# Optimization experiments

Measured on AMD Instinct MI355X. Metric: run time of the kernel, lower is better.

The kernel has to match this reference:

```python
import jax, jax.numpy as jnp
import numpy as np
from jax import lax

K = 3      # kernel_size
C = 64     # n_feat
B, H, W = 2, 256, 256


def _conv(x, w, b, pad):
    # NCHW conv, stride 1
    out = lax.conv_general_dilated(x, w, (1, 1), [(pad, pad), (pad, pad)],
                                   dimension_numbers=('NCHW', 'OIHW', 'NCHW'))
    return out + b[None, :, None, None]


def _prelu(x, a):
    # nn.PReLU() with a single shared learnable slope (init 0.25)
    return jnp.where(x >= 0, x, a * x)


def setup_inputs():
    key = jax.random.key(0)
    ks = jax.random.split(key, 20)
    s = 0.05
    def w(k, shape):
        return jax.random.normal(k, shape, jnp.float32) * s
    inp = {
        'image': jax.random.normal(ks[0], (B, C, H, W), jnp.float32),
        'guidance': jax.random.normal(ks[1], (B, C, H, W), jnp.float32),
        # self.tensor: 1x1 conv (2C -> C) + PReLU (shared with jbf_conv's act)
        'tensor_w': w(ks[2], (C, 2 * C, 1, 1)),
        'tensor_b': jnp.zeros((C,), jnp.float32),
        'a_jbf': jnp.full((1,), 0.25, jnp.float32),
        'kg_w1': w(ks[3], (C, C, 3, 3)), 'kg_b1': jnp.zeros((C,), jnp.float32),
        'kg_w2': w(ks[4], (C, C, 3, 3)), 'kg_b2': jnp.zeros((C,), jnp.float32),
        'kg_w3': w(ks[5], (C, C, 3, 3)), 'kg_b3': jnp.zeros((C,), jnp.float32),
        'kg_w4': w(ks[6], (C, C, 3, 3)), 'kg_b4': jnp.zeros((C,), jnp.float32),
        'kg_w5': w(ks[7], (K * K * C, C, 1, 1)),
        'kg_b5': jnp.zeros((K * K * C,), jnp.float32),
        'a_kg': jnp.full((1,), 0.25, jnp.float32),
        # jbf_conv: 3x3 C->C, PReLU (shared a_jbf), 3x3 C->C
        'jbf_w1': w(ks[8], (C, C, 3, 3)), 'jbf_b1': jnp.zeros((C,), jnp.float32),
        'jbf_w2': w(ks[9], (C, C, 3, 3)), 'jbf_b2': jnp.zeros((C,), jnp.float32),
    }
    return inp


def reference(image, guidance, tensor_w, tensor_b, a_jbf,
              kg_w1, kg_b1, kg_w2, kg_b2, kg_w3, kg_b3, kg_w4, kg_b4,
              kg_w5, kg_b5, a_kg, jbf_w1, jbf_b1, jbf_w2, jbf_b2):
    b, c, h, w = image.shape
    # fuse target+guidance features
    t = _prelu(_conv(jnp.concatenate([image, guidance], axis=1), tensor_w, tensor_b, 0), a_jbf)
    # concat_kg: predict per-pixel dynamic kernel (b, K*K*c, h, w)
    y = t
    for wt, bs in ((kg_w1, kg_b1), (kg_w2, kg_b2), (kg_w3, kg_b3), (kg_w4, kg_b4)):
        y = _prelu(_conv(y, wt, bs, 1), a_kg)
    bi_kernel = _conv(y, kg_w5, kg_b5, 0)
    # unfold: torch layout is channel-major (c, ki, kj) along dim 1
    p = (K - 1) // 2
    xp = jnp.pad(image, ((0, 0), (0, 0), (p, p), (p, p)))
    taps = [xp[:, :, i:i + h, j:j + w] for i in range(K) for j in range(K)]
    patch = jnp.stack(taps, axis=2).reshape(b, c * K * K, h, w)
    # NOTE: faithful to source -- (c*K*K) flat layout reinterpreted as (K*K, c)
    jbf = (patch * bi_kernel).reshape(b, K * K, c, h, w).sum(axis=1)
    out = _conv(_prelu(_conv(jbf, jbf_w1, jbf_b1, 1), a_jbf), jbf_w2, jbf_b2, 1)
    return out + image
```

## Files before the change

### kernel.cpp

```cpp
#include <hip/hip_runtime.h>

#define HW 65536

typedef __bf16 bf16x8 __attribute__((ext_vector_type(8)));
typedef float f32x16 __attribute__((ext_vector_type(16)));

__device__ inline unsigned short f2bf(float x) {
    union { float f; unsigned u; } v; v.f = x;
    unsigned r = v.u + 0x7FFF + ((v.u >> 16) & 1);
    return (unsigned short)(r >> 16);
}
__device__ inline float bfhi2f(unsigned u) {
    union { unsigned u; float f; } v; v.u = u & 0xffff0000u; return v.f;
}
__device__ inline float bflo2f(unsigned u) {
    union { unsigned u; float f; } v; v.u = u << 16; return v.f;
}

union FragU { uint4 u; bf16x8 v; };
__device__ inline bf16x8 ld_frag(const uint4* p) { FragU t; t.u = *p; return t.v; }

__global__ __launch_bounds__(256) void k_wprep(
    const float* __restrict__ w0, const float* __restrict__ w1,
    const float* __restrict__ w2, const float* __restrict__ w3,
    const float* __restrict__ w4, const float* __restrict__ w5,
    const float* __restrict__ w5c, const float* __restrict__ tw,
    unsigned short* __restrict__ wT)
{
    int y = blockIdx.y;
    unsigned short* o = wT + (size_t)y * 36864;
    if (y < 6) {
        const float* ws_[6] = {w0, w1, w2, w3, w4, w5};
        const float* w = ws_[y];
        for (int e = blockIdx.x * 256 + threadIdx.x; e < 36864; e += gridDim.x * 256) {
            int tap = e >> 12, oc = (e >> 6) & 63, ic = e & 63;
            o[e] = f2bf(w[(oc * 64 + ic) * 9 + tap]);
        }
    } else if (y == 6) {
        for (int e = blockIdx.x * 256 + threadIdx.x; e < 36864; e += gridDim.x * 256)
            o[e] = f2bf(w5c[e]);
    } else {
        for (int e = blockIdx.x * 256 + threadIdx.x; e < 8192; e += gridDim.x * 256)
            o[e] = f2bf(tw[e]);
    }
}

__global__ __launch_bounds__(256) void k_tr(
    const float* __restrict__ img, const float* __restrict__ gd,
    unsigned short* __restrict__ imgT, unsigned short* __restrict__ gdT)
{
    __shared__ float sT[64 * 66];
    int tid = threadIdx.x;
    int z = blockIdx.y;
    int b = z & 1;
    const float* src = (z >> 1) ? gd : img;
    unsigned short* dst = (z >> 1) ? gdT : imgT;
    int px0 = blockIdx.x * 64;
    size_t sbase = (size_t)b * 64 * HW + px0;

#pragma unroll
    for (int i = 0; i < 4; ++i) {
        int e = i * 256 + tid;
        int ic = e >> 4, seg = e & 15;
        float4 v = *(const float4*)(src + sbase + (size_t)ic * HW + seg * 4);
        float* p = &sT[ic * 66 + seg * 4];
        ((float2*)p)[0] = make_float2(v.x, v.y);
        ((float2*)p)[1] = make_float2(v.z, v.w);
    }
    __syncthreads();

    size_t dbase = (size_t)b * HW * 64 + (size_t)px0 * 64;
#pragma unroll
    for (int k = 0; k < 2; ++k) {
        int idx = k * 256 + tid;
        int px = idx >> 3, u = idx & 7;
        union { uint4 q; unsigned short h[8]; } o;
#pragma unroll
        for (int j = 0; j < 8; ++j)
            o.h[j] = f2bf(sT[(u * 8 + j) * 66 + px]);
        *(uint4*)(dst + dbase + (size_t)px * 64 + u * 8) = o.q;
    }
}

__global__ __launch_bounds__(256, 2) void k_fusem(
    const unsigned short* __restrict__ imgT, const unsigned short* __restrict__ gdT,
    const unsigned short* __restrict__ wTf, const float* __restrict__ bias,
    const float* __restrict__ a, unsigned short* __restrict__ out)
{
    __shared__ __align__(16) char smem[53504];
    uint4* sX = (uint4*)smem;
    uint4* sW = (uint4*)(smem + 36864);
    float* sB = (float*)(smem + 53248);
    unsigned short* sT16 = (unsigned short*)smem;

    int tid = threadIdx.x;
    int wv = tid >> 6, lane = tid & 63;
    int half = lane >> 5, l31 = lane & 31;
    int b = blockIdx.z;
    int y0 = blockIdx.y * 8, x0 = blockIdx.x * 32;
    size_t zbase = (size_t)b * HW * 64;

    for (int ch = tid; ch < 1024; ch += 256) {
        int kg = ch >> 6, oc = ch & 63;
        sW[ch] = ((const uint4*)wTf)[oc * 16 + kg];
    }
    if (tid < 64) sB[tid] = bias[tid];

    f32x16 acc[2][2];
#pragma unroll
    for (int i = 0; i < 2; ++i)
#pragma unroll
        for (int j = 0; j < 2; ++j)
#pragma unroll
            for (int r = 0; r < 16; ++r) acc[i][j][r] = 0.f;

    for (int h = 0; h < 2; ++h) {
        __syncthreads();
        const unsigned short* src = h ? gdT : imgT;
#pragma unroll
        for (int i = 0; i < 8; ++i) {
            int e = i * 256 + tid;
            int px = e >> 3, ig = e & 7;
            int gy = y0 + (px >> 5), gx = x0 + (px & 31);
            uint4 v = *(const uint4*)(src + zbase + ((size_t)(gy * 256 + gx)) * 64 + ig * 8);
            sX[px * 9 + ig] = v;
        }
        __syncthreads();
#pragma unroll
        for (int c = 0; c < 4; ++c) {
            int ig = c * 2 + half;
            int kg = h * 8 + ig;
            bf16x8 a0 = ld_frag(&sW[kg * 64 + l31]);
            bf16x8 a1 = ld_frag(&sW[kg * 64 + 32 + l31]);
            int p0 = wv * 64 + l31;
            bf16x8 b0 = ld_frag(&sX[p0 * 9 + ig]);
            bf16x8 b1 = ld_frag(&sX[(p0 + 32) * 9 + ig]);
            acc[0][0] = __builtin_amdgcn_mfma_f32_32x32x16_bf16(a0, b0, acc[0][0], 0, 0, 0);
            acc[0][1] = __builtin_amdgcn_mfma_f32_32x32x16_bf16(a0, b1, acc[0][1], 0, 0, 0);
            acc[1][0] = __builtin_amdgcn_mfma_f32_32x32x16_bf16(a1, b0, acc[1][0], 0, 0, 0);
            acc[1][1] = __builtin_amdgcn_mfma_f32_32x32x16_bf16(a1, b1, acc[1][1], 0, 0, 0);
        }
    }

    float slope = a[0];
    __syncthreads();
#pragma unroll
    for (int ot = 0; ot < 2; ++ot)
#pragma unroll
        for (int pt = 0; pt < 2; ++pt) {
            int px = wv * 64 + pt * 32 + l31;
#pragma unroll
            for (int q2 = 0; q2 < 4; ++q2) {
                unsigned short hw[4];
#pragma unroll
                for (int j = 0; j < 4; ++j) {
                    int r = (q2 << 2) | j;
                    int oc = ot * 32 + j + 8 * q2 + 4 * half;
                    float v = acc[ot][pt][r] + sB[oc];
                    v = (v >= 0.f) ? v : slope * v;
                    hw[j] = f2bf(v);
                }
                int unit = ot * 4 + q2;
                int up = unit ^ (px & 7);
                uint2* p = (uint2*)&sT16[px * 64 + up * 8 + half * 4];
                *p = make_uint2((unsigned)hw[0] | ((unsigned)hw[1] << 16),
                                (unsigned)hw[2] | ((unsigned)hw[3] << 16));
            }
        }
    __syncthreads();
#pragma unroll
    for (int k = 0; k < 8; ++k) {
        int col = tid >> 3, u = tid & 7;
        int px = k * 32 + col;
        uint4 v = *(uint4*)&sT16[px * 64 + (u ^ (px & 7)) * 8];
        *(uint4*)(out + zbase + ((size_t)((y0 + k) * 256 + x0 + col)) * 64 + u * 8) = v;
    }
}

#define XU 5

template<int MODE>
__global__ __launch_bounds__(256, 2) void k_conv3m(
    const unsigned short* __restrict__ in, const unsigned short* __restrict__ wT,
    const float* __restrict__ bias, const float* __restrict__ a,
    const float* __restrict__ res, void* __restrict__ outv)
{
    __shared__ __align__(16) char smem[63040];
    uint4* sX = (uint4*)smem;
    uint4* sW = (uint4*)(smem + 25920);
    float* sB = (float*)(smem + 62784);
    unsigned short* sT16 = (unsigned short*)smem;

    int tid = threadIdx.x;
    int wv = tid >> 6, lane = tid & 63;
    int half = lane >> 5, l31 = lane & 31;
    int b = blockIdx.z;
    int y0 = blockIdx.y * 16, x0 = blockIdx.x * 16;
    const size_t zbase = (size_t)b * HW * 64;

    if (tid < 64) sB[tid] = bias[tid];

    f32x16 acc[2][2];
#pragma unroll
    for (int i = 0; i < 2; ++i)
#pragma unroll
        for (int j = 0; j < 2; ++j)
#pragma unroll
            for (int r = 0; r < 16; ++r) acc[i][j][r] = 0.f;

    for (int h = 0; h < 2; ++h) {
        __syncthreads();
#pragma unroll
        for (int i = 0; i < 6; ++i) {
            int e = i * 256 + tid;
            if (e < 1296) {
                int cell = e >> 2, ig = e & 3;
                int r = cell / 18, c = cell - r * 18;
                int gy = y0 + r - 1, gx = x0 + c - 1;
                uint4 v = make_uint4(0, 0, 0, 0);
                if (gy >= 0 && gy < 256 && gx >= 0 && gx < 256)
                    v = *(const uint4*)(in + zbase + ((size_t)(gy * 256 + gx)) * 64 + h * 32 + ig * 8);
                sX[cell * XU + ig] = v;
            }
        }
        for (int ch = tid; ch < 2304; ch += 256) {
            int oc = ch & 63, tg = ch >> 6;
            int ig = tg & 3, tap = tg >> 2;
            sW[ch] = *(const uint4*)(wT + tap * 4096 + oc * 64 + h * 32 + ig * 8);
        }
        __syncthreads();

#pragma unroll
        for (int tap = 0; tap < 9; ++tap) {
            int dy = tap / 3, dx = tap % 3;
#pragma unroll
            for (int c = 0; c < 2; ++c) {
                int ig = c * 2 + half;
                bf16x8 a0 = ld_frag(&sW[(tap * 4 + ig) * 64 + l31]);
                bf16x8 a1 = ld_frag(&sW[(tap * 4 + ig) * 64 + 32 + l31]);
                int p0 = wv * 64 + l31;
                int p1 = p0 + 32;
                int u0 = ((((p0 >> 4) + dy) * 18) + (p0 & 15) + dx) * XU + ig;
                int u1 = ((((p1 >> 4) + dy) * 18) + (p1 & 15) + dx) * XU + ig;
                bf16x8 b0 = ld_frag(&sX[u0]);
                bf16x8 b1 = ld_frag(&sX[u1]);
                acc[0][0] = __builtin_amdgcn_mfma_f32_32x32x16_bf16(a0, b0, acc[0][0], 0, 0, 0);
                acc[0][1] = __builtin_amdgcn_mfma_f32_32x32x16_bf16(a0, b1, acc[0][1], 0, 0, 0);
                acc[1][0] = __builtin_amdgcn_mfma_f32_32x32x16_bf16(a1, b0, acc[1][0], 0, 0, 0);
                acc[1][1] = __builtin_amdgcn_mfma_f32_32x32x16_bf16(a1, b1, acc[1][1], 0, 0, 0);
            }
        }
    }

    if (MODE == 0) {
        float slope = a[0];
        __syncthreads();
#pragma unroll
        for (int ot = 0; ot < 2; ++ot)
#pragma unroll
            for (int pt = 0; pt < 2; ++pt) {
                int px = wv * 64 + pt * 32 + l31;
#pragma unroll
                for (int q2 = 0; q2 < 4; ++q2) {
                    unsigned short hw[4];
#pragma unroll
                    for (int j = 0; j < 4; ++j) {
                        int r = (q2 << 2) | j;
                        int oc = ot * 32 + j + 8 * q2 + 4 * half;
                        float v = acc[ot][pt][r] + sB[oc];
                        v = (v >= 0.f) ? v : slope * v;
                        hw[j] = f2bf(v);
                    }
                    int unit = ot * 4 + q2;
                    int up = unit ^ (px & 7);
                    uint2* p = (uint2*)&sT16[px * 64 + up * 8 + half * 4];
                    *p = make_uint2((unsigned)hw[0] | ((unsigned)hw[1] << 16),
                                    (unsigned)hw[2] | ((unsigned)hw[3] << 16));
                }
            }
        __syncthreads();
        unsigned short* outT = (unsigned short*)outv;
#pragma unroll
        for (int k = 0; k < 8; ++k) {
            int idx = k * 256 + tid;
            int row = idx >> 7, rem = idx & 127;
            int col = rem >> 3, u = rem & 7;
            int px = row * 16 + col;
            uint4 v = *(uint4*)&sT16[px * 64 + (u ^ (px & 7)) * 8];
            *(uint4*)(outT + zbase + ((size_t)((y0 + row) * 256 + x0 + col)) * 64 + u * 8) = v;
        }
    } else {
        float* outF = (float*)outv;
#pragma unroll
        for (int ot = 0; ot < 2; ++ot)
#pragma unroll
            for (int pt = 0; pt < 2; ++pt) {
                int p = wv * 64 + pt * 32 + l31;
                int y = y0 + (p >> 4), x = x0 + (p & 15);
                size_t pbase = (size_t)b * 64 * HW + (size_t)y * 256 + x;
#pragma unroll
                for (int r = 0; r < 16; ++r) {
                    int oc = ot * 32 + (r & 3) + 8 * (r >> 2) + 4 * half;
                    float v = acc[ot][pt][r] + sB[oc];
                    v += res[pbase + (size_t)oc * HW];
                    outF[pbase + (size_t)oc * HW] = v;
                }
            }
    }
}

struct OffTab { unsigned v[9][32]; int chlo[9]; };
constexpr OffTab make_tab() {
    OffTab t{};
    for (int kk = 0; kk < 9; ++kk) {
        int chlo = (kk * 64) / 9;
        t.chlo[kk] = chlo;
        for (int ot = 0; ot < 2; ++ot)
            for (int r = 0; r < 16; ++r) {
                int cc0 = ot * 32 + (r & 3) + 8 * (r >> 2);
                int q0 = kk * 64 + cc0, q1 = q0 + 4;
                int o0 = (q0 / 9 - chlo) * 360 + (q0 % 9 / 3) * 40 + (q0 % 9 % 3);
                int o1 = (q1 / 9 - chlo) * 360 + (q1 % 9 / 3) * 40 + (q1 % 9 % 3);
                t.v[kk][ot * 16 + r] = (unsigned)o0 | ((unsigned)o1 << 16);
            }
    }
    return t;
}
__constant__ OffTab kOff = make_tab();

__global__ __launch_bounds__(256, 2) void k_jbfm(
    const unsigned short* __restrict__ y4, const float* __restrict__ img,
    const unsigned short* __restrict__ w5T, const float* __restrict__ b5,
    unsigned short* __restrict__ out)
{
    __shared__ __align__(16) char smem[78592];
    uint4* sY = (uint4*)smem;
    float* sB5 = (float*)(smem + 76288);
    unsigned short* sT16 = (unsigned short*)smem;

    int tid = threadIdx.x;
    int wv = tid >> 6, lane = tid & 63;
    int half = lane >> 5, l31 = lane & 31;
    int b = blockIdx.z;
    int y0 = blockIdx.y * 8, x0 = blockIdx.x * 32;
    size_t zbase = (size_t)b * HW * 64;
    size_t ibase = (size_t)b * 64 * HW;

    int p_off[3], p_dst[3];
    bool p_a[3], p_b[3], p_act[3];
#pragma unroll
    for (int i = 0; i < 3; ++i) {
        int e = i * 256 + tid;
        bool act = e < 720;
        int ch = e / 90, rem = e - ch * 90;
        int rp = rem / 10, seg = rem - rp * 10;
        int gy = y0 + rp - 1;
        int gxb = x0 - 4 + seg * 4;
        bool xok = (gxb >= 0 && gxb < 256);
        p_act[i] = act;
        p_a[i] = act && xok && gy >= 0 && gy < 256;
        p_b[i] = act && xok && (gy + 1) < 256;
        p_off[i] = ch * HW + gy * 256 + gxb;
        p_dst[i] = ch * 360 + rp * 40 + seg * 4;
    }

#pragma unroll
    for (int i = 0; i < 8; ++i) {
        int e = i * 256 + tid;
        int px = e >> 3, ig = e & 7;
        int gy = y0 + (px >> 5), gx = x0 + (px & 31);
        sY[px * 9 + ig] = *(const uint4*)(y4 + zbase + ((size_t)(gy * 256 + gx)) * 64 + ig * 8);
    }
    for (int e = tid; e < 576; e += 256) sB5[e] = b5[e];

    {
        uint4* sW50 = (uint4*)(smem + 36864);
        unsigned* sP0 = (unsigned*)(smem + 53248);
#pragma unroll
        for (int u = 0; u < 2; ++u) {
            int uu = u * 256 + tid;
            int cc = uu & 63, ig = uu >> 6;
            sW50[uu] = ((const uint4*)w5T)[cc * 8 + ig];
        }
        const float* rp0 = img + ibase;
#pragma unroll
        for (int i = 0; i < 3; ++i) {
            float4 fa = make_float4(0, 0, 0, 0), fb = make_float4(0, 0, 0, 0);
            if (p_a[i]) fa = *(const float4*)(rp0 + p_off[i]);
            if (p_b[i]) fb = *(const float4*)(rp0 + p_off[i] + 256);
            if (p_act[i]) {
                uint4 pk;
                pk.x = (unsigned)f2bf(fa.x) | ((unsigned)f2bf(fb.x) << 16);
                pk.y = (unsigned)f2bf(fa.y) | ((unsigned)f2bf(fb.y) << 16);
                pk.z = (unsigned)f2bf(fa.z) | ((unsigned)f2bf(fb.z) << 16);
                pk.w = (unsigned)f2bf(fa.w) | ((unsigned)f2bf(fb.w) << 16);
                *(uint4*)&sP0[p_dst[i]] = pk;
            }
        }
    }

    float jb[2][2][16];
#pragma unroll
    for (int i = 0; i < 2; ++i)
#pragma unroll
        for (int j = 0; j < 2; ++j)
#pragma unroll
            for (int r = 0; r < 16; ++r) jb[i][j][r] = 0.f;

    __syncthreads();

#pragma unroll 1
    for (int kk = 0; kk < 9; ++kk) {
        const int cur = kk & 1;
        const uint4* sW5c = (const uint4*)(smem + 36864 + cur * 8192);
        const unsigned* sPc = (const unsigned*)(smem + 53248 + cur * 11520);

        uint4 wpre0, wpre1;
        float4 pfa[3], pfb[3];
        if (kk < 8) {
            const int nk = kk + 1;
            const int chlo_n = kOff.chlo[nk];
            {
                int cc = tid & 63, ig = tid >> 6;
                wpre0 = ((const uint4*)w5T)[(nk * 64 + cc) * 8 + ig];
                int uu = 256 + tid;
                int cc1 = uu & 63, ig1 = uu >> 6;
                wpre1 = ((const uint4*)w5T)[(nk * 64 + cc1) * 8 + ig1];
            }
            const float* rp0 = img + ibase + (size_t)chlo_n * HW;
#pragma unroll
            for (int i = 0; i < 3; ++i) {
                pfa[i] = make_float4(0, 0, 0, 0);
                pfb[i] = make_float4(0, 0, 0, 0);
                if (p_a[i]) pfa[i] = *(const float4*)(rp0 + p_off[i]);
                if (p_b[i]) pfb[i] = *(const float4*)(rp0 + p_off[i] + 256);
            }
        }

        f32x16 acc[2][2];
#pragma unroll
        for (int ot = 0; ot < 2; ++ot)
#pragma unroll
            for (int r = 0; r < 16; ++r) {
                int cc0 = ot * 32 + (r & 3) + 8 * (r >> 2);
                float bv = sB5[kk * 64 + cc0 + 4 * half];
                acc[ot][0][r] = bv;
                acc[ot][1][r] = bv;
            }

#pragma unroll
        for (int c = 0; c < 4; ++c) {
            int ig = c * 2 + half;
            bf16x8 a0 = ld_frag(&sW5c[ig * 64 + l31]);
            bf16x8 a1 = ld_frag(&sW5c[ig * 64 + 32 + l31]);
            int p0 = wv * 64 + l31;
            bf16x8 b0 = ld_frag(&sY[p0 * 9 + ig]);
            bf16x8 b1 = ld_frag(&sY[(p0 + 32) * 9 + ig]);
            acc[0][0] = __builtin_amdgcn_mfma_f32_32x32x16_bf16(a0, b0, acc[0][0], 0, 0, 0);
            acc[0][1] = __builtin_amdgcn_mfma_f32_32x32x16_bf16(a0, b1, acc[0][1], 0, 0, 0);
            acc[1][0] = __builtin_amdgcn_mfma_f32_32x32x16_bf16(a1, b0, acc[1][0], 0, 0, 0);
            acc[1][1] = __builtin_amdgcn_mfma_f32_32x32x16_bf16(a1, b1, acc[1][1], 0, 0, 0);
        }

        {
            const unsigned* basep = sPc + wv * 80 + l31 + 3;
            const unsigned* tab = kOff.v[kk];
#pragma unroll
            for (int ot = 0; ot < 2; ++ot)
#pragma unroll
                for (int r = 0; r < 16; ++r) {
                    unsigned oo = tab[ot * 16 + r];
                    unsigned o0 = oo & 0xffffu, o1 = oo >> 16;
                    unsigned pv = basep[half ? o1 : o0];
                    jb[ot][0][r] = fmaf(acc[ot][0][r], bflo2f(pv), jb[ot][0][r]);
                    jb[ot][1][r] = fmaf(acc[ot][1][r], bfhi2f(pv), jb[ot][1][r]);
                }
        }

        if (kk < 8) {
            uint4* sW5n = (uint4*)(smem + 36864 + (cur ^ 1) * 8192);
            unsigned* sPn = (unsigned*)(smem + 53248 + (cur ^ 1) * 11520);
            sW5n[tid] = wpre0;
            sW5n[256 + tid] = wpre1;
#pragma unroll
            for (int i = 0; i < 3; ++i) {
                if (p_act[i]) {
                    uint4 pk;
                    pk.x = (unsigned)f2bf(pfa[i].x) | ((unsigned)f2bf(pfb[i].x) << 16);
                    pk.y = (unsigned)f2bf(pfa[i].y) | ((unsigned)f2bf(pfb[i].y) << 16);
                    pk.z = (unsigned)f2bf(pfa[i].z) | ((unsigned)f2bf(pfb[i].z) << 16);
                    pk.w = (unsigned)f2bf(pfa[i].w) | ((unsigned)f2bf(pfb[i].w) << 16);
                    *(uint4*)&sPn[p_dst[i]] = pk;
                }
            }
        }
        __syncthreads();
    }

#pragma unroll
    for (int ot = 0; ot < 2; ++ot)
#pragma unroll
        for (int pt = 0; pt < 2; ++pt) {
            int px = wv * 64 + pt * 32 + l31;
#pragma unroll
            for (int q2 = 0; q2 < 4; ++q2) {
                unsigned short hw[4];
#pragma unroll
                for (int j = 0; j < 4; ++j) {
                    int r = (q2 << 2) | j;
                    hw[j] = f2bf(jb[ot][pt][r]);
                }
                int unit = ot * 4 + q2;
                int up = unit ^ (px & 7);
                uint2* p = (uint2*)&sT16[px * 64 + up * 8 + half * 4];
                *p = make_uint2((unsigned)hw[0] | ((unsigned)hw[1] << 16),
                                (unsigned)hw[2] | ((unsigned)hw[3] << 16));
            }
        }
    __syncthreads();
#pragma unroll
    for (int k = 0; k < 8; ++k) {
        int col = tid >> 3, u = tid & 7;
        int px = k * 32 + col;
        uint4 v = *(uint4*)&sT16[px * 64 + (u ^ (px & 7)) * 8];
        *(uint4*)(out + zbase + ((size_t)((y0 + k) * 256 + x0 + col)) * 64 + u * 8) = v;
    }
}

extern "C" void kernel_launch(void* const* d_in, const int* in_sizes, int n_in,
                              void* d_out, int out_size, void* d_ws, size_t ws_size,
                              hipStream_t stream) {
    const float* img  = (const float*)d_in[0];
    const float* gd   = (const float*)d_in[1];
    const float* tw   = (const float*)d_in[2];
    const float* tb   = (const float*)d_in[3];
    const float* ajbf = (const float*)d_in[4];
    const float* kw1  = (const float*)d_in[5];
    const float* kb1  = (const float*)d_in[6];
    const float* kw2  = (const float*)d_in[7];
    const float* kb2  = (const float*)d_in[8];
    const float* kw3  = (const float*)d_in[9];
    const float* kb3  = (const float*)d_in[10];
    const float* kw4  = (const float*)d_in[11];
    const float* kb4  = (const float*)d_in[12];
    const float* kw5  = (const float*)d_in[13];
    const float* kb5  = (const float*)d_in[14];
    const float* akg  = (const float*)d_in[15];
    const float* jw1  = (const float*)d_in[16];
    const float* jb1  = (const float*)d_in[17];
    const float* jw2  = (const float*)d_in[18];
    const float* jb2  = (const float*)d_in[19];
    float* out  = (float*)d_out;

    const size_t TEN = (size_t)2 * HW * 64;
    unsigned short* bufA = (unsigned short*)d_ws;
    unsigned short* imgT = bufA + TEN;
    unsigned short* gdT  = imgT + TEN;
    unsigned short* wT   = gdT + TEN;
    unsigned short* bufB = (unsigned short*)d_out;

    dim3 g3(16, 16, 2);
    dim3 gw(8, 32, 2);

    k_tr<<<dim3(1024, 4), 256, 0, stream>>>(img, gd, imgT, gdT);
    k_wprep<<<dim3(4, 8), 256, 0, stream>>>(kw1, kw2, kw3, kw4, jw1, jw2, kw5, tw, wT);

    k_fusem<<<gw, 256, 0, stream>>>(imgT, gdT, wT + (size_t)7 * 36864, tb, ajbf, bufA);

    k_conv3m<0><<<g3, 256, 0, stream>>>(bufA, wT + (size_t)0 * 36864, kb1, akg, nullptr, bufB);
    k_conv3m<0><<<g3, 256, 0, stream>>>(bufB, wT + (size_t)1 * 36864, kb2, akg, nullptr, bufA);
    k_conv3m<0><<<g3, 256, 0, stream>>>(bufA, wT + (size_t)2 * 36864, kb3, akg, nullptr, bufB);
    k_conv3m<0><<<g3, 256, 0, stream>>>(bufB, wT + (size_t)3 * 36864, kb4, akg, nullptr, bufA);

    k_jbfm<<<gw, 256, 0, stream>>>(bufA, img, wT + (size_t)6 * 36864, kb5, bufB);

    k_conv3m<0><<<g3, 256, 0, stream>>>(bufB, wT + (size_t)4 * 36864, jb1, ajbf, nullptr, bufA);
    k_conv3m<2><<<g3, 256, 0, stream>>>(bufA, wT + (size_t)5 * 36864, jb2, ajbf, img, out);
}
```

Measured before the change: 313.6 us.

## Read conv weights directly from global and prefetch second input half into registers

Weights are prelaid out in fragment order so the 3x3 conv and the fused 1x1 kernel load their A fragments straight from global/L2 instead of staging them in LDS. The conv kernel double-buffers the two channel halves in LDS and issues the second half's global loads before computing the first. The fuse kernel prefetches guidance into registers. This cuts LDS footprint and barriers, and lets global latency overlap MFMA work, at the cost of more global weight traffic and register pressure.

Measured after the change: 338.7 us. +8.0%, slower.

```diff
diff --git a/kernel.cpp b/kernel.cpp
--- a/kernel.cpp
+++ b/kernel.cpp
@@ -34,14 +34,19 @@
         const float* w = ws_[y];
         for (int e = blockIdx.x * 256 + threadIdx.x; e < 36864; e += gridDim.x * 256) {
             int tap = e >> 12, oc = (e >> 6) & 63, ic = e & 63;
-            o[e] = f2bf(w[(oc * 64 + ic) * 9 + tap]);
+            int h = ic >> 5, ig = (ic >> 3) & 3, j = ic & 7;
+            int dst = ((h * 2304) + (tap * 4 + ig) * 64 + oc) * 8 + j;
+            o[dst] = f2bf(w[(oc * 64 + ic) * 9 + tap]);
         }
     } else if (y == 6) {
         for (int e = blockIdx.x * 256 + threadIdx.x; e < 36864; e += gridDim.x * 256)
             o[e] = f2bf(w5c[e]);
     } else {
-        for (int e = blockIdx.x * 256 + threadIdx.x; e < 8192; e += gridDim.x * 256)
-            o[e] = f2bf(tw[e]);
+        for (int e = blockIdx.x * 256 + threadIdx.x; e < 8192; e += gridDim.x * 256) {
+            int oc = e >> 7, ic = e & 127;
+            int kg = ic >> 3, j = ic & 7;
+            o[((kg * 64 + oc) << 3) + j] = f2bf(tw[e]);
+        }
     }
 }
 
@@ -87,10 +92,9 @@
     const unsigned short* __restrict__ wTf, const float* __restrict__ bias,
     const float* __restrict__ a, unsigned short* __restrict__ out)
 {
-    __shared__ __align__(16) char smem[53504];
+    __shared__ __align__(16) char smem[37120];
     uint4* sX = (uint4*)smem;
-    uint4* sW = (uint4*)(smem + 36864);
-    float* sB = (float*)(smem + 53248);
+    float* sB = (float*)(smem + 36864);
     unsigned short* sT16 = (unsigned short*)smem;
 
     int tid = threadIdx.x;
@@ -99,11 +103,8 @@
     int b = blockIdx.z;
     int y0 = blockIdx.y * 8, x0 = blockIdx.x * 32;
     size_t zbase = (size_t)b * HW * 64;
-
-    for (int ch = tid; ch < 1024; ch += 256) {
-        int kg = ch >> 6, oc = ch & 63;
-        sW[ch] = ((const uint4*)wTf)[oc * 16 + kg];
-    }
+    const uint4* wg = (const uint4*)wTf;
+
     if (tid < 64) sB[tid] = bias[tid];
 
     f32x16 acc[2][2];
@@ -114,24 +115,29 @@
 #pragma unroll
             for (int r = 0; r < 16; ++r) acc[i][j][r] = 0.f;
 
-    for (int h = 0; h < 2; ++h) {
-        __syncthreads();
-        const unsigned short* src = h ? gdT : imgT;
+    auto loadX = [&](const unsigned short* src, uint4* rx) {
 #pragma unroll
         for (int i = 0; i < 8; ++i) {
             int e = i * 256 + tid;
             int px = e >> 3, ig = e & 7;
             int gy = y0 + (px >> 5), gx = x0 + (px & 31);
-            uint4 v = *(const uint4*)(src + zbase + ((size_t)(gy * 256 + gx)) * 64 + ig * 8);
-            sX[px * 9 + ig] = v;
-        }
-        __syncthreads();
+            rx[i] = *(const uint4*)(src + zbase + ((size_t)(gy * 256 + gx)) * 64 + ig * 8);
+        }
+    };
+    auto writeX = [&](const uint4* rx) {
+#pragma unroll
+        for (int i = 0; i < 8; ++i) {
+            int e = i * 256 + tid;
+            sX[(e >> 3) * 9 + (e & 7)] = rx[i];
+        }
+    };
+    auto compute = [&](int h) {
 #pragma unroll
         for (int c = 0; c < 4; ++c) {
             int ig = c * 2 + half;
             int kg = h * 8 + ig;
-            bf16x8 a0 = ld_frag(&sW[kg * 64 + l31]);
-            bf16x8 a1 = ld_frag(&sW[kg * 64 + 32 + l31]);
+            bf16x8 a0 = ld_frag(&wg[kg * 64 + l31]);
+            bf16x8 a1 = ld_frag(&wg[kg * 64 + 32 + l31]);
             int p0 = wv * 64 + l31;
             bf16x8 b0 = ld_frag(&sX[p0 * 9 + ig]);
             bf16x8 b1 = ld_frag(&sX[(p0 + 32) * 9 + ig]);
@@ -140,7 +146,18 @@
             acc[1][0] = __builtin_amdgcn_mfma_f32_32x32x16_bf16(a1, b0, acc[1][0], 0, 0, 0);
             acc[1][1] = __builtin_amdgcn_mfma_f32_32x32x16_bf16(a1, b1, acc[1][1], 0, 0, 0);
         }
-    }
+    };
+
+    uint4 rx[8], ry[8];
+    loadX(imgT, rx);
+    writeX(rx);
+    loadX(gdT, ry);
+    __syncthreads();
+    compute(0);
+    __syncthreads();
+    writeX(ry);
+    __syncthreads();
+    compute(1);
 
     float slope = a[0];
     __syncthreads();
@@ -185,10 +202,10 @@
     const float* __restrict__ bias, const float* __restrict__ a,
     const float* __restrict__ res, void* __restrict__ outv)
 {
-    __shared__ __align__(16) char smem[63040];
-    uint4* sX = (uint4*)smem;
-    uint4* sW = (uint4*)(smem + 25920);
-    float* sB = (float*)(smem + 62784);
+    __shared__ __align__(16) char smem[52096];
+    uint4* sX0 = (uint4*)smem;
+    uint4* sX1 = (uint4*)(smem + 25920);
+    float* sB = (float*)(smem + 51840);
     unsigned short* sT16 = (unsigned short*)smem;
 
     int tid = threadIdx.x;
@@ -197,6 +214,7 @@
     int b = blockIdx.z;
     int y0 = blockIdx.y * 16, x0 = blockIdx.x * 16;
     const size_t zbase = (size_t)b * HW * 64;
+    const uint4* wg = (const uint4*)wT;
 
     if (tid < 64) sB[tid] = bias[tid];
 
@@ -208,49 +226,57 @@
 #pragma unroll
             for (int r = 0; r < 16; ++r) acc[i][j][r] = 0.f;
 
-    for (int h = 0; h < 2; ++h) {
-        __syncthreads();
+    auto loadX = [&](int h, uint4* rx) {
 #pragma unroll
         for (int i = 0; i < 6; ++i) {
             int e = i * 256 + tid;
-            if (e < 1296) {
-                int cell = e >> 2, ig = e & 3;
-                int r = cell / 18, c = cell - r * 18;
-                int gy = y0 + r - 1, gx = x0 + c - 1;
-                uint4 v = make_uint4(0, 0, 0, 0);
-                if (gy >= 0 && gy < 256 && gx >= 0 && gx < 256)
-                    v = *(const uint4*)(in + zbase + ((size_t)(gy * 256 + gx)) * 64 + h * 32 + ig * 8);
-                sX[cell * XU + ig] = v;
-            }
-        }
-        for (int ch = tid; ch < 2304; ch += 256) {
-            int oc = ch & 63, tg = ch >> 6;
-            int ig = tg & 3, tap = tg >> 2;
-            sW[ch] = *(const uint4*)(wT + tap * 4096 + oc * 64 + h * 32 + ig * 8);
-        }
-        __syncthreads();
-
+            int cell = e >> 2, ig = e & 3;
+            int r = cell / 18, c2 = cell - r * 18;
+            int gy = y0 + r - 1, gx = x0 + c2 - 1;
+            rx[i] = make_uint4(0, 0, 0, 0);
+            if (e < 1296 && gy >= 0 && gy < 256 && gx >= 0 && gx < 256)
+                rx[i] = *(const uint4*)(in + zbase + ((size_t)(gy * 256 + gx)) * 64 + h * 32 + ig * 8);
+        }
+    };
+    auto writeX = [&](uint4* sXd, const uint4* rx) {
+#pragma unroll
+        for (int i = 0; i < 6; ++i) {
+            int e = i * 256 + tid;
+            if (e < 1296) sXd[(e >> 2) * XU + (e & 3)] = rx[i];
+        }
+    };
+    auto compute = [&](int h, const uint4* sXp) {
 #pragma unroll
         for (int tap = 0; tap < 9; ++tap) {
             int dy = tap / 3, dx = tap % 3;
 #pragma unroll
             for (int c = 0; c < 2; ++c) {
                 int ig = c * 2 + half;
-                bf16x8 a0 = ld_frag(&sW[(tap * 4 + ig) * 64 + l31]);
-                bf16x8 a1 = ld_frag(&sW[(tap * 4 + ig) * 64 + 32 + l31]);
+                bf16x8 a0 = ld_frag(&wg[h * 2304 + (tap * 4 + ig) * 64 + l31]);
+                bf16x8 a1 = ld_frag(&wg[h * 2304 + (tap * 4 + ig) * 64 + 32 + l31]);
                 int p0 = wv * 64 + l31;
                 int p1 = p0 + 32;
                 int u0 = ((((p0 >> 4) + dy) * 18) + (p0 & 15) + dx) * XU + ig;
                 int u1 = ((((p1 >> 4) + dy) * 18) + (p1 & 15) + dx) * XU + ig;
-                bf16x8 b0 = ld_frag(&sX[u0]);
-                bf16x8 b1 = ld_frag(&sX[u1]);
+                bf16x8 b0 = ld_frag(&sXp[u0]);
+                bf16x8 b1 = ld_frag(&sXp[u1]);
                 acc[0][0] = __builtin_amdgcn_mfma_f32_32x32x16_bf16(a0, b0, acc[0][0], 0, 0, 0);
                 acc[0][1] = __builtin_amdgcn_mfma_f32_32x32x16_bf16(a0, b1, acc[0][1], 0, 0, 0);
                 acc[1][0] = __builtin_amdgcn_mfma_f32_32x32x16_bf16(a1, b0, acc[1][0], 0, 0, 0);
                 acc[1][1] = __builtin_amdgcn_mfma_f32_32x32x16_bf16(a1, b1, acc[1][1], 0, 0, 0);
             }
         }
-    }
+    };
+
+    uint4 rx[6];
+    loadX(0, rx);
+    writeX(sX0, rx);
+    __syncthreads();
+    loadX(1, rx);
+    compute(0, sX0);
+    writeX(sX1, rx);
+    __syncthreads();
+    compute(1, sX1);
 
     if (MODE == 0) {
         float slope = a[0];
```
